# Kernel optimization log

Measured on AMD Instinct MI355X. Metric: run time of the kernel, lower is better.

Reference implementation:

```python
import jax, jax.numpy as jnp
import numpy as np

N_NODES = 50000
N_EDGES = 800000
N_FEAT = 256
HIDDEN = 128
N_CLASSES = 40


def gcn_conv(x, src, dst, W, b, n_nodes):
    """PyG GCNConv: add self-loops, symmetric normalization, x@W then scatter-add."""
    h = x @ W  # [N, out]
    loop = jnp.arange(n_nodes, dtype=src.dtype)
    s = jnp.concatenate([src, loop])  # [E+N]
    d = jnp.concatenate([dst, loop])
    deg = jax.ops.segment_sum(jnp.ones_like(d, dtype=h.dtype), d, num_segments=n_nodes)
    dinv = jnp.where(deg > 0, jax.lax.rsqrt(deg), 0.0)
    norm = dinv[s] * dinv[d]  # [E+N]
    msg = h[s] * norm[:, None]  # gather + scale
    out = jax.ops.segment_sum(msg, d, num_segments=n_nodes)  # scatter-add to targets
    return out + b


def setup_inputs() -> dict:
    key = jax.random.key(0)
    k1, k2, k3, k4 = jax.random.split(key, 4)
    x = jax.random.normal(k1, (N_NODES, N_FEAT), dtype=jnp.float32)
    edge_index = jax.random.randint(k2, (2, N_EDGES), 0, N_NODES, dtype=jnp.int32)
    # Glorot-style init for conv weights, zero bias (PyG default)
    W1 = jax.random.normal(k3, (N_FEAT, HIDDEN), dtype=jnp.float32) * (1.0 / np.sqrt(N_FEAT))
    b1 = jnp.zeros((HIDDEN,), dtype=jnp.float32)
    W2 = jax.random.normal(k4, (HIDDEN, N_CLASSES), dtype=jnp.float32) * (1.0 / np.sqrt(HIDDEN))
    b2 = jnp.zeros((N_CLASSES,), dtype=jnp.float32)
    return {"x": x, "edge_index": edge_index, "W1": W1, "b1": b1, "W2": W2, "b2": b2}


def reference(x, edge_index, W1, b1, W2, b2):
    # eval mode: dropout is identity
    src, dst = edge_index[0], edge_index[1]
    h = gcn_conv(x, src, dst, W1, b1, N_NODES)
    h = jax.nn.relu(h)
    h = gcn_conv(h, src, dst, W2, b2, N_NODES)
    return jax.nn.log_softmax(h, axis=1)
```

## Files before the change

### kernel.cpp

```cpp
#include <hip/hip_runtime.h>
#include <hip/hip_fp16.h>
#include <cstdint>

#define N_NODES 50000
#define N_EDGES 800000
#define N_FEAT 256
#define HIDDEN 128
#define N_CLASSES 40
#define NBUCKET 196
#define EPB 3125
#define BCAP 8192
#define ROWS_PAD 50048
#define G1_BLOCKS 782
#define H2S 40

typedef _Float16 half8 __attribute__((ext_vector_type(8)));
typedef __fp16 fp16x2 __attribute__((ext_vector_type(2)));
typedef __attribute__((ext_vector_type(4))) float f32x4;

__device__ inline ushort f2h(float f) {
    return __half_as_ushort(__float2half_rn(f));
}
__device__ inline __half2 u2h2(uint u) {
    union { uint u; __half2 h; } v; v.u = u; return v.h;
}

__device__ inline uint wrep(uint u) {
    uint t = u >> 16;
    return (t << 16) | t;
}


__global__ __launch_bounds__(256) void partition_repack(
        const int* __restrict__ src, const int* __restrict__ dst,
        int* __restrict__ cursor, uint* __restrict__ ebuf,
        const float* __restrict__ W1, ushort* __restrict__ Bp1,
        const float* __restrict__ W2, ushort* __restrict__ Bp2) {
    __shared__ int h[NBUCKET];
    __shared__ int base[NBUCKET];
    __shared__ int cur[NBUCKET];
    int blk = blockIdx.x, t = threadIdx.x;
    int gid = blk * 256 + t;
    if (gid < 32768) {
        int j = gid & 7, lane = (gid >> 3) & 63, kt = (gid >> 9) & 7, nt = gid >> 12;
        int k = kt * 32 + (lane >> 4) * 8 + j;
        int n = nt * 16 + (lane & 15);
        Bp1[gid] = f2h(W1[k * HIDDEN + n]);
    } else if (gid < 32768 + 6144) {
        int i2 = gid - 32768;
        int j = i2 & 7, lane = (i2 >> 3) & 63, kt = (i2 >> 9) & 3, nt = i2 >> 11;
        int k = kt * 32 + (lane >> 4) * 8 + j;
        int n = nt * 16 + (lane & 15);
        Bp2[i2] = (n < N_CLASSES) ? f2h(W2[k * N_CLASSES + n]) : (ushort)0;
    }
    if (t < NBUCKET) { h[t] = 0; cur[t] = 0; }
    __syncthreads();
    int eb = blk * EPB;
    for (int i = t; i < EPB; i += 256)
        atomicAdd(&h[dst[eb + i] >> 8], 1);
    __syncthreads();
    if (t < NBUCKET)
        base[t] = (h[t] > 0) ? atomicAdd(&cursor[t], h[t]) : 0;
    __syncthreads();
    for (int i = t; i < EPB; i += 256) {
        int d = dst[eb + i], sv = src[eb + i];
        int bk = d >> 8;
        int p = base[bk] + atomicAdd(&cur[bk], 1);
        ebuf[bk * BCAP + p] = ((uint)d << 16) | (uint)sv;
    }
}


__global__ __launch_bounds__(256) void csr_gemm1(
        const uint* __restrict__ ebuf, const int* __restrict__ cursor,
        int* __restrict__ deg, float* __restrict__ dinv,
        int* __restrict__ rowptr, int* __restrict__ esrc,
        const float* __restrict__ x, const ushort* __restrict__ Bp,
        ushort* __restrict__ h1h) {
    if (blockIdx.x < NBUCKET) {
        __shared__ int s[256];
        __shared__ int cnt[256];
        __shared__ int exc[256];
        __shared__ int cur[256];
        int b = blockIdx.x, t = threadIdx.x;
        s[t] = (t < NBUCKET) ? cursor[t] : 0;
        __syncthreads();
        for (int off = 1; off < 256; off <<= 1) {
            int t2 = 0;
            if (t >= off) t2 = s[t - off];
            __syncthreads();
            s[t] += t2;
            __syncthreads();
        }
        int beg = (b > 0) ? s[b - 1] : 0;
        int ecnt = s[b] - beg;
        __syncthreads();
        cnt[t] = 0;
        cur[t] = 0;
        __syncthreads();
        const uint* eb = ebuf + (size_t)b * BCAP;
        for (int i = t; i < ecnt; i += 256)
            atomicAdd(&cnt[(eb[i] >> 16) & 255], 1);
        __syncthreads();
        int d = cnt[t];
        s[t] = d;
        __syncthreads();
        for (int off = 1; off < 256; off <<= 1) {
            int t2 = 0;
            if (t >= off) t2 = s[t - off];
            __syncthreads();
            s[t] += t2;
            __syncthreads();
        }
        exc[t] = s[t] - d;
        int node = b * 256 + t;
        if (node < N_NODES) {
            deg[node] = d;
            dinv[node] = rsqrtf((float)(d + 1));
            rowptr[node] = beg + exc[t];
        }
        __syncthreads();
        for (int i = t; i < ecnt; i += 256) {
            uint u = eb[i];
            int dl = (int)(u >> 16) & 255;
            int pos = beg + exc[dl] + atomicAdd(&cur[dl], 1);
            esrc[pos] = (int)(u & 0xffffu);
        }
    } else {
        int t = threadIdx.x;
        int lane = t & 63, w = t >> 6;
        int r = lane & 15, q = lane >> 4;
        int row0 = (blockIdx.x - NBUCKET) * 64;
        int arow = row0 + w * 16 + r;
        if (arow >= N_NODES) arow = N_NODES - 1;
        const float* xrow = x + (size_t)arow * N_FEAT;
        f32x4 acc[8] = {};
        for (int kt = 0; kt < 8; ++kt) {
            float4 v0 = *(const float4*)(xrow + kt * 32 + q * 8);
            float4 v1 = *(const float4*)(xrow + kt * 32 + q * 8 + 4);
            union { fp16x2 p[4]; half8 a; } u;
            u.p[0] = __builtin_amdgcn_cvt_pkrtz(v0.x, v0.y);
            u.p[1] = __builtin_amdgcn_cvt_pkrtz(v0.z, v0.w);
            u.p[2] = __builtin_amdgcn_cvt_pkrtz(v1.x, v1.y);
            u.p[3] = __builtin_amdgcn_cvt_pkrtz(v1.z, v1.w);
#pragma unroll
            for (int nt = 0; nt < 8; ++nt) {
                half8 b = *(const half8*)(Bp + (((nt * 8 + kt) * 64) + lane) * 8);
                acc[nt] = __builtin_amdgcn_mfma_f32_16x16x32_f16(u.a, b, acc[nt], 0, 0, 0);
            }
        }
#pragma unroll
        for (int nt = 0; nt < 8; ++nt) {
            int col = nt * 16 + r;
#pragma unroll
            for (int reg = 0; reg < 4; ++reg) {
                int row = row0 + w * 16 + q * 4 + reg;
                if (row < N_NODES) h1h[(size_t)row * HIDDEN + col] = f2h(acc[nt][reg]);
            }
        }
    }
}


__global__ __launch_bounds__(256) void agg1_w2(
        const int* __restrict__ rowptr, const int* __restrict__ deg,
        const int* __restrict__ esrc, const float* __restrict__ dinv,
        const ushort* __restrict__ h1h, const float* __restrict__ b1,
        const ushort* __restrict__ Bp2, ushort* __restrict__ h2h) {
    int w = threadIdx.x >> 6, lane = threadIdx.x & 63;
    int v = blockIdx.x * 4 + w;
    int q = lane >> 4, l = lane & 15;
    int beg = rowptr[v], d = deg[v];
    float dv = dinv[v];
    __half2 z = __float2half2_rn(0.f);
    __half2 c0 = z, c1 = z, c2 = z, c3 = z;
    __half2 e0 = z, e1 = z, e2 = z, e3 = z;
    if (q == 0) {
        uint4 hv = *(const uint4*)(h1h + (size_t)v * HIDDEN + l * 8);
        __half2 gs = __float2half2_rn(dv * dv);
        c0 = __hfma2(u2h2(hv.x), gs, c0);
        c1 = __hfma2(u2h2(hv.y), gs, c1);
        c2 = __hfma2(u2h2(hv.z), gs, c2);
        c3 = __hfma2(u2h2(hv.w), gs, c3);
    }
    int e_l = (lane < d) ? esrc[beg + lane] : 0;
    float wd = (lane < d) ? dinv[e_l] * dv : 0.f;
    int up = (int)(((uint)f2h(wd) << 16) | (uint)e_l);
    int dm = min(d, 64);
    int i = 0;
    for (; i + 16 <= dm; i += 16) {
        int u0 = __shfl(up, i + q, 64);
        int u1 = __shfl(up, i + 4 + q, 64);
        int u2 = __shfl(up, i + 8 + q, 64);
        int u3 = __shfl(up, i + 12 + q, 64);
        int s0 = u0 & 0xffff, s1 = u1 & 0xffff, s2 = u2 & 0xffff, s3 = u3 & 0xffff;
        __half2 gh0 = u2h2(wrep((uint)u0));
        __half2 gh1 = u2h2(wrep((uint)u1));
        __half2 gh2 = u2h2(wrep((uint)u2));
        __half2 gh3 = u2h2(wrep((uint)u3));
        uint4 h0 = *(const uint4*)(h1h + (size_t)s0 * HIDDEN + l * 8);
        uint4 h1 = *(const uint4*)(h1h + (size_t)s1 * HIDDEN + l * 8);
        uint4 h2 = *(const uint4*)(h1h + (size_t)s2 * HIDDEN + l * 8);
        uint4 h3 = *(const uint4*)(h1h + (size_t)s3 * HIDDEN + l * 8);
        c0 = __hfma2(u2h2(h0.x), gh0, c0);
        c1 = __hfma2(u2h2(h0.y), gh0, c1);
        c2 = __hfma2(u2h2(h0.z), gh0, c2);
        c3 = __hfma2(u2h2(h0.w), gh0, c3);
        e0 = __hfma2(u2h2(h1.x), gh1, e0);
        e1 = __hfma2(u2h2(h1.y), gh1, e1);
        e2 = __hfma2(u2h2(h1.z), gh1, e2);
        e3 = __hfma2(u2h2(h1.w), gh1, e3);
        c0 = __hfma2(u2h2(h2.x), gh2, c0);
        c1 = __hfma2(u2h2(h2.y), gh2, c1);
        c2 = __hfma2(u2h2(h2.z), gh2, c2);
        c3 = __hfma2(u2h2(h2.w), gh2, c3);
        e0 = __hfma2(u2h2(h3.x), gh3, e0);
        e1 = __hfma2(u2h2(h3.y), gh3, e1);
        e2 = __hfma2(u2h2(h3.z), gh3, e2);
        e3 = __hfma2(u2h2(h3.w), gh3, e3);
    }
    for (; i + 8 <= dm; i += 8) {
        int u0 = __shfl(up, i + q, 64);
        int u1 = __shfl(up, i + 4 + q, 64);
        int s0 = u0 & 0xffff, s1 = u1 & 0xffff;
        __half2 gh0 = u2h2(wrep((uint)u0));
        __half2 gh1 = u2h2(wrep((uint)u1));
        uint4 h0 = *(const uint4*)(h1h + (size_t)s0 * HIDDEN + l * 8);
        uint4 h1 = *(const uint4*)(h1h + (size_t)s1 * HIDDEN + l * 8);
        c0 = __hfma2(u2h2(h0.x), gh0, c0);
        c1 = __hfma2(u2h2(h0.y), gh0, c1);
        c2 = __hfma2(u2h2(h0.z), gh0, c2);
        c3 = __hfma2(u2h2(h0.w), gh0, c3);
        e0 = __hfma2(u2h2(h1.x), gh1, e0);
        e1 = __hfma2(u2h2(h1.y), gh1, e1);
        e2 = __hfma2(u2h2(h1.z), gh1, e2);
        e3 = __hfma2(u2h2(h1.w), gh1, e3);
    }
    for (; i < dm; i += 4) {
        int idx = i + q;
        int cl = idx & 63;
        int u0 = __shfl(up, cl, 64);
        int s0 = u0 & 0xffff;
        __half2 gh0 = u2h2(wrep((uint)u0));
        if (idx >= dm) gh0 = z;
        uint4 h0 = *(const uint4*)(h1h + (size_t)s0 * HIDDEN + l * 8);
        c0 = __hfma2(u2h2(h0.x), gh0, c0);
        c1 = __hfma2(u2h2(h0.y), gh0, c1);
        c2 = __hfma2(u2h2(h0.z), gh0, c2);
        c3 = __hfma2(u2h2(h0.w), gh0, c3);
    }
    for (int j = 64 + q; j < d; j += 4) {
        int s = esrc[beg + j];
        __half2 g = __float2half2_rn(dinv[s] * dv);
        uint4 hs = *(const uint4*)(h1h + (size_t)s * HIDDEN + l * 8);
        c0 = __hfma2(u2h2(hs.x), g, c0);
        c1 = __hfma2(u2h2(hs.y), g, c1);
        c2 = __hfma2(u2h2(hs.z), g, c2);
        c3 = __hfma2(u2h2(hs.w), g, c3);
    }
    float2 f0 = __half22float2(c0), f1 = __half22float2(c1);
    float2 f2 = __half22float2(c2), f3 = __half22float2(c3);
    float2 g0 = __half22float2(e0), g1 = __half22float2(e1);
    float2 g2 = __half22float2(e2), g3 = __half22float2(e3);
    float a0 = f0.x + g0.x, a1 = f0.y + g0.y;
    float a2 = f1.x + g1.x, a3 = f1.y + g1.y;
    float a4 = f2.x + g2.x, a5 = f2.y + g2.y;
    float a6 = f3.x + g3.x, a7 = f3.y + g3.y;
    a0 += __shfl_xor(a0, 16, 64); a0 += __shfl_xor(a0, 32, 64);
    a1 += __shfl_xor(a1, 16, 64); a1 += __shfl_xor(a1, 32, 64);
    a2 += __shfl_xor(a2, 16, 64); a2 += __shfl_xor(a2, 32, 64);
    a3 += __shfl_xor(a3, 16, 64); a3 += __shfl_xor(a3, 32, 64);
    a4 += __shfl_xor(a4, 16, 64); a4 += __shfl_xor(a4, 32, 64);
    a5 += __shfl_xor(a5, 16, 64); a5 += __shfl_xor(a5, 32, 64);
    a6 += __shfl_xor(a6, 16, 64); a6 += __shfl_xor(a6, 32, 64);
    a7 += __shfl_xor(a7, 16, 64); a7 += __shfl_xor(a7, 32, 64);
    float4 bb0 = ((const float4*)b1)[l * 2];
    float4 bb1 = ((const float4*)b1)[l * 2 + 1];
    a0 += bb0.x; a1 += bb0.y; a2 += bb0.z; a3 += bb0.w;
    a4 += bb1.x; a5 += bb1.y; a6 += bb1.z; a7 += bb1.w;
    a0 = a0 > 0.f ? a0 : 0.f;  a1 = a1 > 0.f ? a1 : 0.f;
    a2 = a2 > 0.f ? a2 : 0.f;  a3 = a3 > 0.f ? a3 : 0.f;
    a4 = a4 > 0.f ? a4 : 0.f;  a5 = a5 > 0.f ? a5 : 0.f;
    a6 = a6 > 0.f ? a6 : 0.f;  a7 = a7 > 0.f ? a7 : 0.f;
    uint pk0 = ((uint)f2h(a1) << 16) | (uint)f2h(a0);
    uint pk1 = ((uint)f2h(a3) << 16) | (uint)f2h(a2);
    uint pk2 = ((uint)f2h(a5) << 16) | (uint)f2h(a4);
    uint pk3 = ((uint)f2h(a7) << 16) | (uint)f2h(a6);
    f32x4 acc[3] = {};
#pragma unroll
    for (int kt = 0; kt < 4; ++kt) {
        int srcl = kt * 4 + q;
        union { uint u[4]; half8 a; } ua;
        ua.u[0] = (uint)__shfl((int)pk0, srcl, 64);
        ua.u[1] = (uint)__shfl((int)pk1, srcl, 64);
        ua.u[2] = (uint)__shfl((int)pk2, srcl, 64);
        ua.u[3] = (uint)__shfl((int)pk3, srcl, 64);
#pragma unroll
        for (int nt = 0; nt < 3; ++nt) {
            half8 b = *(const half8*)(Bp2 + (((nt * 4 + kt) * 64) + lane) * 8);
            acc[nt] = __builtin_amdgcn_mfma_f32_16x16x32_f16(ua.a, b, acc[nt], 0, 0, 0);
        }
    }
    if (q == 0) {
        h2h[(size_t)v * H2S + l] = f2h(acc[0][0]);
    } else if (q == 1) {
        h2h[(size_t)v * H2S + 16 + l] = f2h(acc[1][0]);
    } else if (q == 2 && l < 8) {
        h2h[(size_t)v * H2S + 32 + l] = f2h(acc[2][0]);
    }
}


__global__ __launch_bounds__(256) void agg2_lsm(
        const int* __restrict__ rowptr, const int* __restrict__ deg,
        const int* __restrict__ esrc, const float* __restrict__ dinv,
        const ushort* __restrict__ h2h, const float* __restrict__ b2,
        float* __restrict__ out) {
    int t = threadIdx.x;
    int w = t >> 6, lane = t & 63;
    int half = lane >> 5, l = lane & 31;
    int v = blockIdx.x * 8 + w * 2 + half;
    int beg = rowptr[v], d = deg[v];
    float dv = dinv[v];
    __half2 z = __float2half2_rn(0.f);
    __half2 cA = z, cB = z;
    {
        uint hv = *(const uint*)(h2h + (size_t)v * H2S + l * 2);
        cA = __hfma2(u2h2(hv), __float2half2_rn(dv * dv), cA);
    }
    int e_l = (l < d) ? esrc[beg + l] : 0;
    float wd = (l < d) ? dinv[e_l] * dv : 0.f;
    int up = (int)(((uint)f2h(wd) << 16) | (uint)e_l);
    int dm = min(d, 32);
    int base = half * 32;
    int i = 0;
    for (; i + 8 <= dm; i += 8) {
        int u0 = __shfl(up, base + i + 0, 64);
        int u1 = __shfl(up, base + i + 1, 64);
        int u2 = __shfl(up, base + i + 2, 64);
        int u3 = __shfl(up, base + i + 3, 64);
        int u4 = __shfl(up, base + i + 4, 64);
        int u5 = __shfl(up, base + i + 5, 64);
        int u6 = __shfl(up, base + i + 6, 64);
        int u7 = __shfl(up, base + i + 7, 64);
        uint h0 = *(const uint*)(h2h + (size_t)(u0 & 0xffff) * H2S + l * 2);
        uint h1 = *(const uint*)(h2h + (size_t)(u1 & 0xffff) * H2S + l * 2);
        uint h2 = *(const uint*)(h2h + (size_t)(u2 & 0xffff) * H2S + l * 2);
        uint h3 = *(const uint*)(h2h + (size_t)(u3 & 0xffff) * H2S + l * 2);
        uint h4 = *(const uint*)(h2h + (size_t)(u4 & 0xffff) * H2S + l * 2);
        uint h5 = *(const uint*)(h2h + (size_t)(u5 & 0xffff) * H2S + l * 2);
        uint h6 = *(const uint*)(h2h + (size_t)(u6 & 0xffff) * H2S + l * 2);
        uint h7 = *(const uint*)(h2h + (size_t)(u7 & 0xffff) * H2S + l * 2);
        cA = __hfma2(u2h2(h0), u2h2(wrep((uint)u0)), cA);
        cB = __hfma2(u2h2(h1), u2h2(wrep((uint)u1)), cB);
        cA = __hfma2(u2h2(h2), u2h2(wrep((uint)u2)), cA);
        cB = __hfma2(u2h2(h3), u2h2(wrep((uint)u3)), cB);
        cA = __hfma2(u2h2(h4), u2h2(wrep((uint)u4)), cA);
        cB = __hfma2(u2h2(h5), u2h2(wrep((uint)u5)), cB);
        cA = __hfma2(u2h2(h6), u2h2(wrep((uint)u6)), cA);
        cB = __hfma2(u2h2(h7), u2h2(wrep((uint)u7)), cB);
    }
    for (; i + 4 <= dm; i += 4) {
        int u0 = __shfl(up, base + i + 0, 64);
        int u1 = __shfl(up, base + i + 1, 64);
        int u2 = __shfl(up, base + i + 2, 64);
        int u3 = __shfl(up, base + i + 3, 64);
        uint h0 = *(const uint*)(h2h + (size_t)(u0 & 0xffff) * H2S + l * 2);
        uint h1 = *(const uint*)(h2h + (size_t)(u1 & 0xffff) * H2S + l * 2);
        uint h2 = *(const uint*)(h2h + (size_t)(u2 & 0xffff) * H2S + l * 2);
        uint h3 = *(const uint*)(h2h + (size_t)(u3 & 0xffff) * H2S + l * 2);
        cA = __hfma2(u2h2(h0), u2h2(wrep((uint)u0)), cA);
        cB = __hfma2(u2h2(h1), u2h2(wrep((uint)u1)), cB);
        cA = __hfma2(u2h2(h2), u2h2(wrep((uint)u2)), cA);
        cB = __hfma2(u2h2(h3), u2h2(wrep((uint)u3)), cB);
    }
    for (; i < dm; ++i) {
        int u0 = __shfl(up, base + i, 64);
        uint h0 = *(const uint*)(h2h + (size_t)(u0 & 0xffff) * H2S + l * 2);
        cA = __hfma2(u2h2(h0), u2h2(wrep((uint)u0)), cA);
    }
    for (i = 32; i < d; ++i) {
        int s = esrc[beg + i];
        float g = dinv[s] * dv;
        uint hs = *(const uint*)(h2h + (size_t)s * H2S + l * 2);
        cA = __hfma2(u2h2(hs), __float2half2_rn(g), cA);
    }
    float2 fA = __half22float2(cA);
    float2 fB = __half22float2(cB);
    float ax = fA.x + fB.x, ay = fA.y + fB.y;
    if (l < 20) {
        float2 bb = ((const float2*)b2)[l];
        ax += bb.x; ay += bb.y;
    }
    float m = (l < 20) ? fmaxf(ax, ay) : -INFINITY;
#pragma unroll
    for (int off = 16; off; off >>= 1) m = fmaxf(m, __shfl_xor(m, off, 64));
    float e = (l < 20) ? (expf(ax - m) + expf(ay - m)) : 0.f;
#pragma unroll
    for (int off = 16; off; off >>= 1) e += __shfl_xor(e, off, 64);
    float ls = logf(e);
    if (l < 20) {
        float2 o;
        o.x = ax - m - ls;
        o.y = ay - m - ls;
        ((float2*)(out + (size_t)v * N_CLASSES))[l] = o;
    }
}


extern "C" void kernel_launch(void* const* d_in, const int* in_sizes, int n_in,
                              void* d_out, int out_size, void* d_ws, size_t ws_size,
                              hipStream_t stream) {
    const float* x  = (const float*)d_in[0];
    const int*   ei = (const int*)d_in[1];
    const float* W1 = (const float*)d_in[2];
    const float* b1 = (const float*)d_in[3];
    const float* W2 = (const float*)d_in[4];
    const float* b2 = (const float*)d_in[5];
    const int* src = ei;
    const int* dst = ei + N_EDGES;
    float* out = (float*)d_out;

    char* ws = (char*)d_ws;
    size_t off = 0;
    auto alloc = [&](size_t bytes) {
        void* p = ws + off;
        off += (bytes + 255) & ~(size_t)255;
        return p;
    };
    int*    cursor = (int*)alloc((size_t)NBUCKET * 4);
    int*    deg    = (int*)alloc((size_t)N_NODES * 4);
    float*  dinv   = (float*)alloc((size_t)N_NODES * 4);
    int*    rowptr = (int*)alloc((size_t)N_NODES * 4);
    uint*   ebuf   = (uint*)alloc((size_t)NBUCKET * BCAP * 4);
    int*    esrc   = (int*)alloc((size_t)N_EDGES * 4);
    ushort* Bp1    = (ushort*)alloc((size_t)32768 * 2);
    ushort* Bp2    = (ushort*)alloc((size_t)6144 * 2);
    ushort* h1h    = (ushort*)alloc((size_t)ROWS_PAD * HIDDEN * 2);
    ushort* h2h    = (ushort*)alloc((size_t)ROWS_PAD * H2S * 2);

    (void)hipMemsetAsync(cursor, 0, (size_t)NBUCKET * 4, stream);
    partition_repack<<<256, 256, 0, stream>>>(src, dst, cursor, ebuf, W1, Bp1, W2, Bp2);

    csr_gemm1<<<NBUCKET + G1_BLOCKS, 256, 0, stream>>>(
        ebuf, cursor, deg, dinv, rowptr, esrc, x, Bp1, h1h);

    agg1_w2<<<N_NODES / 4, 256, 0, stream>>>(rowptr, deg, esrc, dinv, h1h, b1, Bp2, h2h);

    agg2_lsm<<<N_NODES / 8, 256, 0, stream>>>(rowptr, deg, esrc, dinv, h2h, b2, out);
}
```

Baseline: 189.6 us.

## Map one node per quarter-wave in agg1 and batch W2 MFMA over 16 nodes

The first aggregation now gives each 16-lane quarter-wave its own destination node, so a block handles 16 nodes instead of 4. This drops the cross-quarter shuffle reduction and reads edge lists in chunks of 16. Aggregated rows are staged in LDS, and three waves run full 16-row MFMA tiles for the W2 projection, where before only one row of each tile was useful. The h2 row stride is padded to 64. The cost is load imbalance: every quarter-wave loops to the largest degree among the four nodes sharing its wave, plus one added block barrier.

```diff
diff --git a/kernel.cpp b/kernel.cpp
--- a/kernel.cpp
+++ b/kernel.cpp
@@ -12,7 +12,8 @@
 #define BCAP 8192
 #define ROWS_PAD 50048
 #define G1_BLOCKS 782
-#define H2S 40
+#define H2S 64
+#define LROW 136
 
 typedef _Float16 half8 __attribute__((ext_vector_type(8)));
 typedef __fp16 fp16x2 __attribute__((ext_vector_type(2)));
@@ -24,7 +25,6 @@
 __device__ inline __half2 u2h2(uint u) {
     union { uint u; __half2 h; } v; v.u = u; return v.h;
 }
-
 __device__ inline uint wrep(uint u) {
     uint t = u >> 16;
     return (t << 16) | t;
@@ -167,146 +167,104 @@
         const int* __restrict__ esrc, const float* __restrict__ dinv,
         const ushort* __restrict__ h1h, const float* __restrict__ b1,
         const ushort* __restrict__ Bp2, ushort* __restrict__ h2h) {
-    int w = threadIdx.x >> 6, lane = threadIdx.x & 63;
-    int v = blockIdx.x * 4 + w;
-    int q = lane >> 4, l = lane & 15;
+    __shared__ ushort hag[16 * LROW];
+    int t = threadIdx.x;
+    int w = t >> 6, lane = t & 63;
+    int q = lane >> 4, l15 = lane & 15;
+    int n = w * 4 + q;
+    int v = blockIdx.x * 16 + n;
     int beg = rowptr[v], d = deg[v];
     float dv = dinv[v];
     __half2 z = __float2half2_rn(0.f);
-    __half2 c0 = z, c1 = z, c2 = z, c3 = z;
-    __half2 e0 = z, e1 = z, e2 = z, e3 = z;
-    if (q == 0) {
-        uint4 hv = *(const uint4*)(h1h + (size_t)v * HIDDEN + l * 8);
+    __half2 cA0 = z, cA1 = z, cA2 = z, cA3 = z;
+    __half2 cB0 = z, cB1 = z, cB2 = z, cB3 = z;
+    {
+        uint4 hv = *(const uint4*)(h1h + (size_t)v * HIDDEN + l15 * 8);
         __half2 gs = __float2half2_rn(dv * dv);
-        c0 = __hfma2(u2h2(hv.x), gs, c0);
-        c1 = __hfma2(u2h2(hv.y), gs, c1);
-        c2 = __hfma2(u2h2(hv.z), gs, c2);
-        c3 = __hfma2(u2h2(hv.w), gs, c3);
-    }
-    int e_l = (lane < d) ? esrc[beg + lane] : 0;
-    float wd = (lane < d) ? dinv[e_l] * dv : 0.f;
-    int up = (int)(((uint)f2h(wd) << 16) | (uint)e_l);
-    int dm = min(d, 64);
-    int i = 0;
-    for (; i + 16 <= dm; i += 16) {
-        int u0 = __shfl(up, i + q, 64);
-        int u1 = __shfl(up, i + 4 + q, 64);
-        int u2 = __shfl(up, i + 8 + q, 64);
-        int u3 = __shfl(up, i + 12 + q, 64);
-        int s0 = u0 & 0xffff, s1 = u1 & 0xffff, s2 = u2 & 0xffff, s3 = u3 & 0xffff;
-        __half2 gh0 = u2h2(wrep((uint)u0));
-        __half2 gh1 = u2h2(wrep((uint)u1));
-        __half2 gh2 = u2h2(wrep((uint)u2));
-        __half2 gh3 = u2h2(wrep((uint)u3));
-        uint4 h0 = *(const uint4*)(h1h + (size_t)s0 * HIDDEN + l * 8);
-        uint4 h1 = *(const uint4*)(h1h + (size_t)s1 * HIDDEN + l * 8);
-        uint4 h2 = *(const uint4*)(h1h + (size_t)s2 * HIDDEN + l * 8);
-        uint4 h3 = *(const uint4*)(h1h + (size_t)s3 * HIDDEN + l * 8);
-        c0 = __hfma2(u2h2(h0.x), gh0, c0);
-        c1 = __hfma2(u2h2(h0.y), gh0, c1);
-        c2 = __hfma2(u2h2(h0.z), gh0, c2);
-        c3 = __hfma2(u2h2(h0.w), gh0, c3);
-        e0 = __hfma2(u2h2(h1.x), gh1, e0);
-        e1 = __hfma2(u2h2(h1.y), gh1, e1);
-        e2 = __hfma2(u2h2(h1.z), gh1, e2);
-        e3 = __hfma2(u2h2(h1.w), gh1, e3);
-        c0 = __hfma2(u2h2(h2.x), gh2, c0);
-        c1 = __hfma2(u2h2(h2.y), gh2, c1);
-        c2 = __hfma2(u2h2(h2.z), gh2, c2);
-        c3 = __hfma2(u2h2(h2.w), gh2, c3);
-        e0 = __hfma2(u2h2(h3.x), gh3, e0);
-        e1 = __hfma2(u2h2(h3.y), gh3, e1);
-        e2 = __hfma2(u2h2(h3.z), gh3, e2);
-        e3 = __hfma2(u2h2(h3.w), gh3, e3);
-    }
-    for (; i + 8 <= dm; i += 8) {
-        int u0 = __shfl(up, i + q, 64);
-        int u1 = __shfl(up, i + 4 + q, 64);
-        int s0 = u0 & 0xffff, s1 = u1 & 0xffff;
-        __half2 gh0 = u2h2(wrep((uint)u0));
-        __half2 gh1 = u2h2(wrep((uint)u1));
-        uint4 h0 = *(const uint4*)(h1h + (size_t)s0 * HIDDEN + l * 8);
-        uint4 h1 = *(const uint4*)(h1h + (size_t)s1 * HIDDEN + l * 8);
-        c0 = __hfma2(u2h2(h0.x), gh0, c0);
-        c1 = __hfma2(u2h2(h0.y), gh0, c1);
-        c2 = __hfma2(u2h2(h0.z), gh0, c2);
-        c3 = __hfma2(u2h2(h0.w), gh0, c3);
-        e0 = __hfma2(u2h2(h1.x), gh1, e0);
-        e1 = __hfma2(u2h2(h1.y), gh1, e1);
-        e2 = __hfma2(u2h2(h1.z), gh1, e2);
-        e3 = __hfma2(u2h2(h1.w), gh1, e3);
-    }
-    for (; i < dm; i += 4) {
-        int idx = i + q;
-        int cl = idx & 63;
-        int u0 = __shfl(up, cl, 64);
-        int s0 = u0 & 0xffff;
-        __half2 gh0 = u2h2(wrep((uint)u0));
-        if (idx >= dm) gh0 = z;
-        uint4 h0 = *(const uint4*)(h1h + (size_t)s0 * HIDDEN + l * 8);
-        c0 = __hfma2(u2h2(h0.x), gh0, c0);
-        c1 = __hfma2(u2h2(h0.y), gh0, c1);
-        c2 = __hfma2(u2h2(h0.z), gh0, c2);
-        c3 = __hfma2(u2h2(h0.w), gh0, c3);
-    }
-    for (int j = 64 + q; j < d; j += 4) {
-        int s = esrc[beg + j];
-        __half2 g = __float2half2_rn(dinv[s] * dv);
-        uint4 hs = *(const uint4*)(h1h + (size_t)s * HIDDEN + l * 8);
-        c0 = __hfma2(u2h2(hs.x), g, c0);
-        c1 = __hfma2(u2h2(hs.y), g, c1);
-        c2 = __hfma2(u2h2(hs.z), g, c2);
-        c3 = __hfma2(u2h2(hs.w), g, c3);
-    }
-    float2 f0 = __half22float2(c0), f1 = __half22float2(c1);
-    float2 f2 = __half22float2(c2), f3 = __half22float2(c3);
-    float2 g0 = __half22float2(e0), g1 = __half22float2(e1);
-    float2 g2 = __half22float2(e2), g3 = __half22float2(e3);
-    float a0 = f0.x + g0.x, a1 = f0.y + g0.y;
-    float a2 = f1.x + g1.x, a3 = f1.y + g1.y;
-    float a4 = f2.x + g2.x, a5 = f2.y + g2.y;
-    float a6 = f3.x + g3.x, a7 = f3.y + g3.y;
-    a0 += __shfl_xor(a0, 16, 64); a0 += __shfl_xor(a0, 32, 64);
-    a1 += __shfl_xor(a1, 16, 64); a1 += __shfl_xor(a1, 32, 64);
-    a2 += __shfl_xor(a2, 16, 64); a2 += __shfl_xor(a2, 32, 64);
-    a3 += __shfl_xor(a3, 16, 64); a3 += __shfl_xor(a3, 32, 64);
-    a4 += __shfl_xor(a4, 16, 64); a4 += __shfl_xor(a4, 32, 64);
-    a5 += __shfl_xor(a5, 16, 64); a5 += __shfl_xor(a5, 32, 64);
-    a6 += __shfl_xor(a6, 16, 64); a6 += __shfl_xor(a6, 32, 64);
-    a7 += __shfl_xor(a7, 16, 64); a7 += __shfl_xor(a7, 32, 64);
-    float4 bb0 = ((const float4*)b1)[l * 2];
-    float4 bb1 = ((const float4*)b1)[l * 2 + 1];
+        cA0 = __hfma2(u2h2(hv.x), gs, cA0);
+        cA1 = __hfma2(u2h2(hv.y), gs, cA1);
+        cA2 = __hfma2(u2h2(hv.z), gs, cA2);
+        cA3 = __hfma2(u2h2(hv.w), gs, cA3);
+    }
+    int dmx = max(d, __shfl_xor(d, 16, 64));
+    dmx = max(dmx, __shfl_xor(dmx, 32, 64));
+    int qb = lane & 48;
+    for (int c = 0; c < dmx; c += 16) {
+        int idx = c + l15;
+        int e = (idx < d) ? esrc[beg + idx] : 0;
+        float wd = (idx < d) ? dinv[e] * dv : 0.f;
+        int up = (int)(((uint)f2h(wd) << 16) | (uint)e);
+        int lim = min(dmx - c, 16);
+        for (int j = 0; j < lim; j += 4) {
+            int u0 = __shfl(up, qb + j + 0, 64);
+            int u1 = __shfl(up, qb + j + 1, 64);
+            int u2 = __shfl(up, qb + j + 2, 64);
+            int u3 = __shfl(up, qb + j + 3, 64);
+            uint4 g0 = *(const uint4*)(h1h + (size_t)(u0 & 0xffff) * HIDDEN + l15 * 8);
+            uint4 g1 = *(const uint4*)(h1h + (size_t)(u1 & 0xffff) * HIDDEN + l15 * 8);
+            uint4 g2 = *(const uint4*)(h1h + (size_t)(u2 & 0xffff) * HIDDEN + l15 * 8);
+            uint4 g3 = *(const uint4*)(h1h + (size_t)(u3 & 0xffff) * HIDDEN + l15 * 8);
+            __half2 w0 = u2h2(wrep((uint)u0));
+            __half2 w1 = u2h2(wrep((uint)u1));
+            __half2 w2 = u2h2(wrep((uint)u2));
+            __half2 w3 = u2h2(wrep((uint)u3));
+            cA0 = __hfma2(u2h2(g0.x), w0, cA0);
+            cA1 = __hfma2(u2h2(g0.y), w0, cA1);
+            cA2 = __hfma2(u2h2(g0.z), w0, cA2);
+            cA3 = __hfma2(u2h2(g0.w), w0, cA3);
+            cB0 = __hfma2(u2h2(g1.x), w1, cB0);
+            cB1 = __hfma2(u2h2(g1.y), w1, cB1);
+            cB2 = __hfma2(u2h2(g1.z), w1, cB2);
+            cB3 = __hfma2(u2h2(g1.w), w1, cB3);
+            cA0 = __hfma2(u2h2(g2.x), w2, cA0);
+            cA1 = __hfma2(u2h2(g2.y), w2, cA1);
+            cA2 = __hfma2(u2h2(g2.z), w2, cA2);
+            cA3 = __hfma2(u2h2(g2.w), w2, cA3);
+            cB0 = __hfma2(u2h2(g3.x), w3, cB0);
+            cB1 = __hfma2(u2h2(g3.y), w3, cB1);
+            cB2 = __hfma2(u2h2(g3.z), w3, cB2);
+            cB3 = __hfma2(u2h2(g3.w), w3, cB3);
+        }
+    }
+    float2 fA0 = __half22float2(cA0), fB0 = __half22float2(cB0);
+    float2 fA1 = __half22float2(cA1), fB1 = __half22float2(cB1);
+    float2 fA2 = __half22float2(cA2), fB2 = __half22float2(cB2);
+    float2 fA3 = __half22float2(cA3), fB3 = __half22float2(cB3);
+    float a0 = fA0.x + fB0.x, a1 = fA0.y + fB0.y;
+    float a2 = fA1.x + fB1.x, a3 = fA1.y + fB1.y;
+    float a4 = fA2.x + fB2.x, a5 = fA2.y + fB2.y;
+    float a6 = fA3.x + fB3.x, a7 = fA3.y + fB3.y;
+    float4 bb0 = ((const float4*)b1)[l15 * 2];
+    float4 bb1 = ((const float4*)b1)[l15 * 2 + 1];
     a0 += bb0.x; a1 += bb0.y; a2 += bb0.z; a3 += bb0.w;
     a4 += bb1.x; a5 += bb1.y; a6 += bb1.z; a7 += bb1.w;
     a0 = a0 > 0.f ? a0 : 0.f;  a1 = a1 > 0.f ? a1 : 0.f;
     a2 = a2 > 0.f ? a2 : 0.f;  a3 = a3 > 0.f ? a3 : 0.f;
     a4 = a4 > 0.f ? a4 : 0.f;  a5 = a5 > 0.f ? a5 : 0.f;
     a6 = a6 > 0.f ? a6 : 0.f;  a7 = a7 > 0.f ? a7 : 0.f;
-    uint pk0 = ((uint)f2h(a1) << 16) | (uint)f2h(a0);
-    uint pk1 = ((uint)f2h(a3) << 16) | (uint)f2h(a2);
-    uint pk2 = ((uint)f2h(a5) << 16) | (uint)f2h(a4);
-    uint pk3 = ((uint)f2h(a7) << 16) | (uint)f2h(a6);
-    f32x4 acc[3] = {};
-#pragma unroll
-    for (int kt = 0; kt < 4; ++kt) {
-        int srcl = kt * 4 + q;
-        union { uint u[4]; half8 a; } ua;
-        ua.u[0] = (uint)__shfl((int)pk0, srcl, 64);
-        ua.u[1] = (uint)__shfl((int)pk1, srcl, 64);
-        ua.u[2] = (uint)__shfl((int)pk2, srcl, 64);
-        ua.u[3] = (uint)__shfl((int)pk3, srcl, 64);
-#pragma unroll
-        for (int nt = 0; nt < 3; ++nt) {
-            half8 b = *(const half8*)(Bp2 + (((nt * 4 + kt) * 64) + lane) * 8);
-            acc[nt] = __builtin_amdgcn_mfma_f32_16x16x32_f16(ua.a, b, acc[nt], 0, 0, 0);
-        }
-    }
-    if (q == 0) {
-        h2h[(size_t)v * H2S + l] = f2h(acc[0][0]);
-    } else if (q == 1) {
-        h2h[(size_t)v * H2S + 16 + l] = f2h(acc[1][0]);
-    } else if (q == 2 && l < 8) {
-        h2h[(size_t)v * H2S + 32 + l] = f2h(acc[2][0]);
+    uint4 ov;
+    ov.x = ((uint)f2h(a1) << 16) | (uint)f2h(a0);
+    ov.y = ((uint)f2h(a3) << 16) | (uint)f2h(a2);
+    ov.z = ((uint)f2h(a5) << 16) | (uint)f2h(a4);
+    ov.w = ((uint)f2h(a7) << 16) | (uint)f2h(a6);
+    *(uint4*)(&hag[n * LROW + l15 * 8]) = ov;
+    __syncthreads();
+    if (w < 3) {
+        int r = lane & 15;
+        f32x4 acc = {};
+#pragma unroll
+        for (int kt = 0; kt < 4; ++kt) {
+            half8 a = *(const half8*)(&hag[r * LROW + kt * 32 + q * 8]);
+            half8 b = *(const half8*)(Bp2 + (((w * 4 + kt) * 64) + lane) * 8);
+            acc = __builtin_amdgcn_mfma_f32_16x16x32_f16(a, b, acc, 0, 0, 0);
+        }
+        int col = w * 16 + r;
+        if (col < N_CLASSES) {
+            int vb = blockIdx.x * 16 + q * 4;
+#pragma unroll
+            for (int reg = 0; reg < 4; ++reg)
+                h2h[(size_t)(vb + reg) * H2S + col] = f2h(acc[reg]);
+        }
     }
 }
 
@@ -445,7 +403,7 @@
     csr_gemm1<<<NBUCKET + G1_BLOCKS, 256, 0, stream>>>(
         ebuf, cursor, deg, dinv, rowptr, esrc, x, Bp1, h1h);
 
-    agg1_w2<<<N_NODES / 4, 256, 0, stream>>>(rowptr, deg, esrc, dinv, h1h, b1, Bp2, h2h);
+    agg1_w2<<<N_NODES / 16, 256, 0, stream>>>(rowptr, deg, esrc, dinv, h1h, b1, Bp2, h2h);
 
     agg2_lsm<<<N_NODES / 8, 256, 0, stream>>>(rowptr, deg, esrc, dinv, h2h, b2, out);
 }
```

Result: faster. 177.2 us (-6.5%).
